# Kernel tuning notes

Measured on AMD Instinct MI355X. Metric: run time of the kernel, lower is better.

Reference implementation:

```python
import jax, jax.numpy as jnp
import numpy as np

C = 1024          # embed_dim
H = 16            # num_heads
D = C // H        # head_dim = 64
M = 64            # memory_size
HID = 4 * C       # mlp hidden
EPS = 1e-5


def _ln(x, g, b):
    mu = jnp.mean(x, axis=-1, keepdims=True)
    var = jnp.mean(jnp.square(x - mu), axis=-1, keepdims=True)
    return (x - mu) * jax.lax.rsqrt(var + EPS) * g + b


def setup_inputs() -> dict:
    key = jax.random.key(0)
    ks = jax.random.split(key, 16)
    s = 0.02
    return {
        'x': jax.random.normal(ks[0], (2, 2048, C), jnp.float32),
        'memory': jax.random.normal(ks[1], (1, M, C), jnp.float32),
        'ln1_g': jnp.ones((C,), jnp.float32),
        'ln1_b': jnp.zeros((C,), jnp.float32),
        'w_qkv': jax.random.normal(ks[2], (C, 3 * C), jnp.float32) * s,
        'b_qkv': jnp.zeros((3 * C,), jnp.float32),
        'w_out': jax.random.normal(ks[3], (C, C), jnp.float32) * s,
        'b_out': jnp.zeros((C,), jnp.float32),
        'w_mem': jax.random.normal(ks[4], (C, C), jnp.float32) * s,
        'b_mem': jnp.zeros((C,), jnp.float32),
        'ln2_g': jnp.ones((C,), jnp.float32),
        'ln2_b': jnp.zeros((C,), jnp.float32),
        'w_fc1': jax.random.normal(ks[5], (C, HID), jnp.float32) * s,
        'b_fc1': jnp.zeros((HID,), jnp.float32),
        'w_fc2': jax.random.normal(ks[6], (HID, C), jnp.float32) * s,
        'b_fc2': jnp.zeros((C,), jnp.float32),
    }


def reference(x, memory, ln1_g, ln1_b, w_qkv, b_qkv, w_out, b_out,
              w_mem, b_mem, ln2_g, ln2_b, w_fc1, b_fc1, w_fc2, b_fc2):
    B, T, _ = x.shape
    scale = 1.0 / np.sqrt(D)

    # --- InfiniAttention on norm1(x) ---
    h = _ln(x, ln1_g, ln1_b)
    qkv = (h @ w_qkv + b_qkv).reshape(B, T, 3, H, D)
    q = qkv[:, :, 0].transpose(0, 2, 1, 3)  # (B,H,T,D)
    k = qkv[:, :, 1].transpose(0, 2, 1, 3)
    v = qkv[:, :, 2].transpose(0, 2, 1, 3)

    # local full softmax attention over the window of T tokens
    attn = jax.nn.softmax(jnp.einsum('bhtd,bhsd->bhts', q, k) * scale, axis=-1)
    local_out = jnp.einsum('bhts,bhsd->bhtd', attn, v)

    # compressive memory read: mem acts as both K and V
    mem = (memory @ w_mem + b_mem)                 # (1,M,C)
    mem_kv = jnp.broadcast_to(mem, (B, M, C)).reshape(B, M, H, D).transpose(0, 2, 1, 3)  # (B,H,M,D)
    mem_attn = jax.nn.softmax(jnp.einsum('bhtd,bhmd->bhtm', q, mem_kv) * scale, axis=-1)
    mem_out = jnp.einsum('bhtm,bhmd->bhtd', mem_attn, mem_kv)

    out = (local_out + mem_out).transpose(0, 2, 1, 3).reshape(B, T, C)
    out = out @ w_out + b_out
    x = x + out

    # --- MLP on norm2(x) ---
    h2 = _ln(x, ln2_g, ln2_b)
    h2 = jax.nn.gelu(h2 @ w_fc1 + b_fc1, approximate=False)
    x = x + h2 @ w_fc2 + b_fc2
    return x
```

## Files before the change

kernel.cpp:

```cpp
#include <hip/hip_runtime.h>
#include <hip/hip_bf16.h>

typedef unsigned short u16;
typedef unsigned int u32;
typedef short bf16x8 __attribute__((ext_vector_type(8)));
typedef float f32x4 __attribute__((ext_vector_type(4)));

__device__ __forceinline__ u16 f2bf(float x) {
    u32 u = __float_as_uint(x);
    u32 rounding = 0x7FFFu + ((u >> 16) & 1u);
    return (u16)((u + rounding) >> 16);
}

__device__ __forceinline__ void gload_lds16(const u16* g, u16* l) {
    __builtin_amdgcn_global_load_lds((const __attribute__((address_space(1))) void*)g,
                                     (__attribute__((address_space(3))) void*)l, 16, 0, 0);
}

__global__ __launch_bounds__(256) void ln_kernel(const float* __restrict__ in,
                                                 const float* __restrict__ g,
                                                 const float* __restrict__ b,
                                                 u16* __restrict__ outp) {
    int tok = blockIdx.x;
    int t = threadIdx.x;
    const float4* row = (const float4*)(in + (size_t)tok * 1024);
    float4 v = row[t];
    float s = v.x + v.y + v.z + v.w;
    float sq = v.x * v.x + v.y * v.y + v.z * v.z + v.w * v.w;
#pragma unroll
    for (int off = 32; off >= 1; off >>= 1) {
        s += __shfl_xor(s, off);
        sq += __shfl_xor(sq, off);
    }
    __shared__ float rs[4], rq[4];
    int lane = t & 63, w = t >> 6;
    if (lane == 0) { rs[w] = s; rq[w] = sq; }
    __syncthreads();
    s = rs[0] + rs[1] + rs[2] + rs[3];
    sq = rq[0] + rq[1] + rq[2] + rq[3];
    float mean = s * (1.0f / 1024.0f);
    float var = sq * (1.0f / 1024.0f) - mean * mean;
    float rstd = rsqrtf(var + 1e-5f);
    float4 gg = ((const float4*)g)[t];
    float4 bb = ((const float4*)b)[t];
    u16* o = outp + (size_t)tok * 1024 + t * 4;
    o[0] = f2bf((v.x - mean) * rstd * gg.x + bb.x);
    o[1] = f2bf((v.y - mean) * rstd * gg.y + bb.y);
    o[2] = f2bf((v.z - mean) * rstd * gg.z + bb.z);
    o[3] = f2bf((v.w - mean) * rstd * gg.w + bb.w);
}

__global__ __launch_bounds__(256) void transpose_w(const float* __restrict__ W,
                                                   u16* __restrict__ WT, int K, int N) {
    __shared__ float tile[32][33];
    int n0 = blockIdx.x * 32, k0 = blockIdx.y * 32;
    int tx = threadIdx.x & 31, ty = threadIdx.x >> 5;
#pragma unroll
    for (int i = 0; i < 4; i++) {
        int kk = ty + i * 8;
        tile[kk][tx] = W[(size_t)(k0 + kk) * N + n0 + tx];
    }
    __syncthreads();
#pragma unroll
    for (int i = 0; i < 4; i++) {
        int nn = ty + i * 8;
        WT[(size_t)(n0 + nn) * K + k0 + tx] = f2bf(tile[tx][nn]);
    }
}

__global__ void convert_bf(const float* __restrict__ in, u16* __restrict__ outp, int n) {
    int i = blockIdx.x * blockDim.x + threadIdx.x;
    if (i < n) outp[i] = f2bf(in[i]);
}

template <int MODE, int BM>
__global__ __launch_bounds__(256) void gemm_bf16(const u16* A, const u16* BT,
                                                 const float* __restrict__ bias,
                                                 const float* res, void* outv,
                                                 int M, int N, int K) {
    __shared__ __align__(16) u16 As[BM * 32];
    __shared__ __align__(16) u16 Bs[128 * 32];
    constexpr int MI = BM / 32;
    int rowBase = blockIdx.y * BM, colBase = blockIdx.x * 128;
    int t = threadIdx.x, lane = t & 63, w = t >> 6;
    int wr = w >> 1, wc = w & 1, r = lane & 15, g = lane >> 4;

    int lrow = lane >> 2;
    int scol = (lane & 3) * 8;
    const u16* b0 = BT + (size_t)(colBase + (w * 2 + 0) * 16 + lrow) * K + scol;
    const u16* b1 = BT + (size_t)(colBase + (w * 2 + 1) * 16 + lrow) * K + scol;
    u16* lB0 = &Bs[(w * 2 + 0) * 512];
    u16* lB1 = &Bs[(w * 2 + 1) * 512];
    const u16* a0;
    const u16* a1 = nullptr;
    u16 *lA0, *lA1 = nullptr;
    if constexpr (BM == 128) {
        a0 = A + (size_t)(rowBase + (w * 2 + 0) * 16 + lrow) * K + scol;
        a1 = A + (size_t)(rowBase + (w * 2 + 1) * 16 + lrow) * K + scol;
        lA0 = &As[(w * 2 + 0) * 512];
        lA1 = &As[(w * 2 + 1) * 512];
    } else {
        a0 = A + (size_t)(rowBase + w * 16 + lrow) * K + scol;
        lA0 = &As[w * 512];
    }

    f32x4 acc[MI][4] = {};

    for (int k0 = 0; k0 < K; k0 += 32) {
        __syncthreads();
        gload_lds16(a0 + k0, lA0);
        if constexpr (BM == 128) gload_lds16(a1 + k0, lA1);
        gload_lds16(b0 + k0, lB0);
        gload_lds16(b1 + k0, lB1);
        __syncthreads();
        bf16x8 af[MI], bfr[4];
#pragma unroll
        for (int mi = 0; mi < MI; mi++)
            af[mi] = *(const bf16x8*)&As[(wr * (BM / 2) + mi * 16 + r) * 32 + g * 8];
#pragma unroll
        for (int ni = 0; ni < 4; ni++)
            bfr[ni] = *(const bf16x8*)&Bs[(wc * 64 + ni * 16 + r) * 32 + g * 8];
#pragma unroll
        for (int mi = 0; mi < MI; mi++)
#pragma unroll
            for (int ni = 0; ni < 4; ni++)
                acc[mi][ni] = __builtin_amdgcn_mfma_f32_16x16x32_bf16(af[mi], bfr[ni], acc[mi][ni], 0, 0, 0);
    }

#pragma unroll
    for (int mi = 0; mi < MI; mi++) {
#pragma unroll
        for (int ni = 0; ni < 4; ni++) {
#pragma unroll
            for (int rr = 0; rr < 4; rr++) {
                int grow = rowBase + wr * (BM / 2) + mi * 16 + g * 4 + rr;
                int gcol = colBase + wc * 64 + ni * 16 + r;
                if (grow < M) {
                    float v = acc[mi][ni][rr] + bias[gcol];
                    if constexpr (MODE == 1) {
                        v = 0.5f * v * (1.0f + erff(v * 0.70710678118f));
                    }
                    if constexpr (MODE == 2) {
                        ((float*)outv)[(size_t)grow * N + gcol] = v + res[(size_t)grow * N + gcol];
                    } else {
                        ((u16*)outv)[(size_t)grow * N + gcol] = f2bf(v);
                    }
                }
            }
        }
    }
}

__global__ __launch_bounds__(256) void attn_kernel(const u16* __restrict__ qkv,
                                                   const u16* __restrict__ memkv,
                                                   u16* __restrict__ outp) {
    __shared__ __align__(16) u16 K_lds[64][72];
    __shared__ __align__(16) u32 P32[64][36];
    __shared__ __align__(16) u32 VT32[64][36];
    const int T = 2048, C3 = 3072;
    int qt = blockIdx.x, bh = blockIdx.y;
    int b = bh >> 4, h = bh & 15;
    int t0 = qt * 64;
    int tid = threadIdx.x, lane = tid & 63, w = tid >> 6, r = lane & 15, g = lane >> 4;
    size_t qkvb = (size_t)b * T * C3;

    const u16* qrow = qkv + qkvb + (size_t)(t0 + w * 16 + r) * C3 + h * 64;
    bf16x8 aq0 = *(const bf16x8*)(qrow + g * 8);
    bf16x8 aq1 = *(const bf16x8*)(qrow + 32 + g * 8);
#pragma unroll
    for (int i = 0; i < 8; i++) {
        float f0 = __uint_as_float(((u32)(u16)aq0[i]) << 16) * 0.18033688f;
        float f1 = __uint_as_float(((u32)(u16)aq1[i]) << 16) * 0.18033688f;
        aq0[i] = (short)f2bf(f0);
        aq1[i] = (short)f2bf(f1);
    }

    int s_row = tid >> 3;
    int s_col = (tid & 7) << 3;
    int v_d = tid & 63;
    int v_u = tid >> 6;

    f32x4 O[4] = {};
    float m_[4] = {-1e30f, -1e30f, -1e30f, -1e30f};
    float lv[4] = {0.f, 0.f, 0.f, 0.f};

    struct VRegs { uint4 k0, k1; u32 va[8]; };

    auto load_tile = [&](const u16* Kb2, size_t Kstr, const u16* Vb2, size_t Vstr) {
        VRegs R;
        R.k0 = *(const uint4*)&Kb2[Kstr * s_row + s_col];
        R.k1 = *(const uint4*)&Kb2[Kstr * (s_row + 32) + s_col];
        const u16* vp = Vb2 + v_d;
#pragma unroll
        for (int j = 0; j < 4; j++) {
            int rv = (j < 2) ? (2 * v_u + j) : (8 + 2 * v_u + (j - 2));
            R.va[2 * j] = (u32)vp[(size_t)rv * Vstr] | ((u32)vp[(size_t)(rv + 16) * Vstr] << 16);
            R.va[2 * j + 1] = (u32)vp[(size_t)(rv + 32) * Vstr] | ((u32)vp[(size_t)(rv + 48) * Vstr] << 16);
        }
        return R;
    };
    auto write_tile = [&](const VRegs& R) {
        *(uint4*)&K_lds[s_row][s_col] = R.k0;
        *(uint4*)&K_lds[s_row + 32][s_col] = R.k1;
        uint4 w0, w1;
        w0.x = R.va[0]; w0.y = R.va[1]; w0.z = R.va[2]; w0.w = R.va[3];
        w1.x = R.va[4]; w1.y = R.va[5]; w1.z = R.va[6]; w1.w = R.va[7];
        *(uint4*)&VT32[v_d][4 * v_u] = w0;
        *(uint4*)&VT32[v_d][16 + 4 * v_u] = w1;
    };

    auto compute_tile = [&]() {
        f32x4 sv[4];
#pragma unroll
        for (int n = 0; n < 4; n++) {
            bf16x8 bk0 = *(const bf16x8*)&K_lds[n * 16 + r][g * 8];
            bf16x8 bk1 = *(const bf16x8*)&K_lds[n * 16 + r][32 + g * 8];
            f32x4 z = {0.f, 0.f, 0.f, 0.f};
            z = __builtin_amdgcn_mfma_f32_16x16x32_bf16(aq0, bk0, z, 0, 0, 0);
            z = __builtin_amdgcn_mfma_f32_16x16x32_bf16(aq1, bk1, z, 0, 0, 0);
            sv[n] = z;
        }
        float mxl[4];
#pragma unroll
        for (int rr = 0; rr < 4; rr++)
            mxl[rr] = fmaxf(fmaxf(sv[0][rr], sv[1][rr]), fmaxf(sv[2][rr], sv[3][rr]));
        float dmax = fmaxf(fmaxf(mxl[0] - m_[0], mxl[1] - m_[1]),
                           fmaxf(mxl[2] - m_[2], mxl[3] - m_[3]));
        if (!__all(dmax <= 8.0f)) {
#pragma unroll
            for (int rr = 0; rr < 4; rr++) {
                float mxr = mxl[rr];
#pragma unroll
                for (int off = 8; off >= 1; off >>= 1) mxr = fmaxf(mxr, __shfl_xor(mxr, off));
                float mn = fmaxf(m_[rr], mxr);
                float alpha = exp2f(m_[rr] - mn);
                m_[rr] = mn;
                lv[rr] *= alpha;
#pragma unroll
                for (int n = 0; n < 4; n++) O[n][rr] *= alpha;
            }
        }
#pragma unroll
        for (int rr = 0; rr < 4; rr++) {
            float p0 = exp2f(sv[0][rr] - m_[rr]);
            float p1 = exp2f(sv[1][rr] - m_[rr]);
            float p2 = exp2f(sv[2][rr] - m_[rr]);
            float p3 = exp2f(sv[3][rr] - m_[rr]);
            lv[rr] += (p0 + p1) + (p2 + p3);
            uint2 pw;
            pw.x = __builtin_amdgcn_perm(__float_as_uint(p1), __float_as_uint(p0), 0x07060302u);
            pw.y = __builtin_amdgcn_perm(__float_as_uint(p3), __float_as_uint(p2), 0x07060302u);
            *(uint2*)&P32[w * 16 + g * 4 + rr][2 * r] = pw;
        }
        bf16x8 ap0 = *(const bf16x8*)&P32[w * 16 + r][4 * g];
        bf16x8 ap1 = *(const bf16x8*)&P32[w * 16 + r][16 + 4 * g];
#pragma unroll
        for (int n = 0; n < 4; n++) {
            bf16x8 bv0 = *(const bf16x8*)&VT32[n * 16 + r][4 * g];
            bf16x8 bv1 = *(const bf16x8*)&VT32[n * 16 + r][16 + 4 * g];
            O[n] = __builtin_amdgcn_mfma_f32_16x16x32_bf16(ap0, bv0, O[n], 0, 0, 0);
            O[n] = __builtin_amdgcn_mfma_f32_16x16x32_bf16(ap1, bv1, O[n], 0, 0, 0);
        }
    };

    const u16* Kb = qkv + qkvb + 1024 + h * 64;
    const u16* Vb = qkv + qkvb + 2048 + h * 64;
    VRegs R = load_tile(Kb, C3, Vb, C3);
    for (int t = 0; t < 32; t++) {
        __syncthreads();
        write_tile(R);
        __syncthreads();
        if (t < 31)
            R = load_tile(Kb + (size_t)(t + 1) * 64 * C3, C3, Vb + (size_t)(t + 1) * 64 * C3, C3);
        else
            R = load_tile(memkv + h * 64, 1024, memkv + h * 64, 1024);
        compute_tile();
    }
    float outLocal[4][4];
#pragma unroll
    for (int rr = 0; rr < 4; rr++) {
        float ls = lv[rr];
#pragma unroll
        for (int off = 8; off >= 1; off >>= 1) ls += __shfl_xor(ls, off);
        float inv = 1.0f / ls;
#pragma unroll
        for (int n = 0; n < 4; n++) outLocal[n][rr] = O[n][rr] * inv;
    }
#pragma unroll
    for (int n = 0; n < 4; n++) { f32x4 z = {0.f, 0.f, 0.f, 0.f}; O[n] = z; }
#pragma unroll
    for (int rr = 0; rr < 4; rr++) { m_[rr] = -1e30f; lv[rr] = 0.f; }
    __syncthreads();
    write_tile(R);
    __syncthreads();
    compute_tile();
#pragma unroll
    for (int rr = 0; rr < 4; rr++) {
        float ls = lv[rr];
#pragma unroll
        for (int off = 8; off >= 1; off >>= 1) ls += __shfl_xor(ls, off);
        float inv = 1.0f / ls;
        int row = t0 + w * 16 + g * 4 + rr;
#pragma unroll
        for (int n = 0; n < 4; n++) {
            float v2 = outLocal[n][rr] + O[n][rr] * inv;
            outp[((size_t)(b * T + row)) * 1024 + h * 64 + n * 16 + r] = f2bf(v2);
        }
    }
}

extern "C" void kernel_launch(void* const* d_in, const int* in_sizes, int n_in,
                              void* d_out, int out_size, void* d_ws, size_t ws_size,
                              hipStream_t stream) {
    const float* x      = (const float*)d_in[0];
    const float* memory = (const float*)d_in[1];
    const float* ln1_g  = (const float*)d_in[2];
    const float* ln1_b  = (const float*)d_in[3];
    const float* w_qkv  = (const float*)d_in[4];
    const float* b_qkv  = (const float*)d_in[5];
    const float* w_out  = (const float*)d_in[6];
    const float* b_out  = (const float*)d_in[7];
    const float* w_mem  = (const float*)d_in[8];
    const float* b_mem  = (const float*)d_in[9];
    const float* ln2_g  = (const float*)d_in[10];
    const float* ln2_b  = (const float*)d_in[11];
    const float* w_fc1  = (const float*)d_in[12];
    const float* b_fc1  = (const float*)d_in[13];
    const float* w_fc2  = (const float*)d_in[14];
    const float* b_fc2  = (const float*)d_in[15];
    float* out = (float*)d_out;

    char* ws = (char*)d_ws;
    size_t off = 0;
    auto alloc = [&](size_t bytes) { size_t o = off; off += (bytes + 255) & ~(size_t)255; return o; };
    u16* h_bf    = (u16*)(ws + alloc((size_t)4096 * 1024 * 2));
    u16* qkv_bf  = (u16*)(ws + alloc((size_t)4096 * 3072 * 2));
    u16* attn_bf = (u16*)(ws + alloc((size_t)4096 * 1024 * 2));
    u16* g1_bf   = (u16*)(ws + alloc((size_t)4096 * 4096 * 2));
    u16* mem_bf  = (u16*)(ws + alloc((size_t)64 * 1024 * 2));
    u16* memA_bf = (u16*)(ws + alloc((size_t)64 * 1024 * 2));
    u16* wqkvT   = (u16*)(ws + alloc((size_t)3072 * 1024 * 2));
    u16* woutT   = (u16*)(ws + alloc((size_t)1024 * 1024 * 2));
    u16* wmemT   = (u16*)(ws + alloc((size_t)1024 * 1024 * 2));
    u16* wfc1T   = (u16*)(ws + alloc((size_t)4096 * 1024 * 2));
    u16* wfc2T   = (u16*)(ws + alloc((size_t)1024 * 4096 * 2));

    transpose_w<<<dim3(3072 / 32, 1024 / 32), 256, 0, stream>>>(w_qkv, wqkvT, 1024, 3072);
    transpose_w<<<dim3(1024 / 32, 1024 / 32), 256, 0, stream>>>(w_out, woutT, 1024, 1024);
    transpose_w<<<dim3(1024 / 32, 1024 / 32), 256, 0, stream>>>(w_mem, wmemT, 1024, 1024);
    transpose_w<<<dim3(4096 / 32, 1024 / 32), 256, 0, stream>>>(w_fc1, wfc1T, 1024, 4096);
    transpose_w<<<dim3(1024 / 32, 4096 / 32), 256, 0, stream>>>(w_fc2, wfc2T, 4096, 1024);
    convert_bf<<<dim3(256), 256, 0, stream>>>(memory, memA_bf, 64 * 1024);

    ln_kernel<<<dim3(4096), 256, 0, stream>>>(x, ln1_g, ln1_b, h_bf);

    gemm_bf16<0, 128><<<dim3(24, 32), 256, 0, stream>>>(h_bf, wqkvT, b_qkv, nullptr, qkv_bf, 4096, 3072, 1024);

    gemm_bf16<0, 64><<<dim3(8, 1), 256, 0, stream>>>(memA_bf, wmemT, b_mem, nullptr, mem_bf, 64, 1024, 1024);

    attn_kernel<<<dim3(32, 32), 256, 0, stream>>>(qkv_bf, mem_bf, attn_bf);

    gemm_bf16<2, 64><<<dim3(8, 64), 256, 0, stream>>>(attn_bf, woutT, b_out, x, out, 4096, 1024, 1024);

    ln_kernel<<<dim3(4096), 256, 0, stream>>>(out, ln2_g, ln2_b, h_bf);

    gemm_bf16<1, 128><<<dim3(32, 32), 256, 0, stream>>>(h_bf, wfc1T, b_fc1, nullptr, g1_bf, 4096, 4096, 1024);

    gemm_bf16<2, 64><<<dim3(8, 64), 256, 0, stream>>>(g1_bf, wfc2T, b_fc2, out, out, 4096, 1024, 4096);

    (void)in_sizes; (void)n_in; (void)out_size; (void)ws_size;
}
```

Measured before the change: 524.2 us.

## Pre-tile K/V into swizzled layout and double-buffer attention via direct LDS loads

Adds a prep_kv kernel that rewrites K and transposed V (and the memory K/V) into per-tile, XOR-swizzled 64x64 blocks, stored in the unused fc1 buffer. The attention kernel then stages each tile with global_load_lds into double-buffered LDS, removing the register round trip and the strided 2-byte V gathers. It also swizzles P and drops one barrier per iteration. An XCD-aware block remap is applied to the GEMMs and attention for L2 locality. The cost is an extra pass over K/V and extra launches.

```diff
diff --git a/kernel.cpp b/kernel.cpp
--- a/kernel.cpp
+++ b/kernel.cpp
@@ -15,6 +15,12 @@
 __device__ __forceinline__ void gload_lds16(const u16* g, u16* l) {
     __builtin_amdgcn_global_load_lds((const __attribute__((address_space(1))) void*)g,
                                      (__attribute__((address_space(3))) void*)l, 16, 0, 0);
+}
+
+__device__ __forceinline__ int xcd_swz(int id, int nwg) {
+    int q = nwg >> 3, r = nwg & 7;
+    int x = id & 7, k = id >> 3;
+    return (x < r ? x * (q + 1) : r * (q + 1) + (x - r) * q) + k;
 }
 
 __global__ __launch_bounds__(256) void ln_kernel(const float* __restrict__ in,
@@ -73,6 +79,40 @@
     if (i < n) outp[i] = f2bf(in[i]);
 }
 
+__global__ __launch_bounds__(256) void prep_kv(const u16* __restrict__ src,
+                                               u32* __restrict__ kdst, u32* __restrict__ vdst,
+                                               long bstride, int rstride, int koff, int voff) {
+    int t = blockIdx.x, bh = blockIdx.y;
+    int b = bh >> 4, h = bh & 15;
+    int tid = threadIdx.x;
+    const u16* kS = src + (size_t)b * bstride + (size_t)(t * 64) * rstride + koff + h * 64;
+    const u16* vS = src + (size_t)b * bstride + (size_t)(t * 64) * rstride + voff + h * 64;
+    u32* kD = kdst + ((size_t)bh * gridDim.x + t) * 2048;
+    u32* vD = vdst + ((size_t)bh * gridDim.x + t) * 2048;
+#pragma unroll
+    for (int c = 0; c < 2; c++) {
+        int idx = tid + c * 256;
+        int row = idx >> 3, blk = idx & 7;
+        uint4 q = *(const uint4*)&kS[(size_t)row * rstride + blk * 8];
+        *(uint4*)&kD[row * 32 + ((blk ^ (row & 7)) << 2)] = q;
+    }
+#pragma unroll
+    for (int c = 0; c < 2; c++) {
+        int idx = tid + c * 256;
+        int drow = idx >> 3, kblk = idx & 7;
+        u32 vv[4];
+#pragma unroll
+        for (int e = 0; e < 4; e++) {
+            int j0 = kblk * 8 + 2 * e, j1 = j0 + 1;
+            int kv0 = 16 * (j0 & 3) + (j0 >> 2);
+            int kv1 = 16 * (j1 & 3) + (j1 >> 2);
+            vv[e] = (u32)vS[(size_t)kv0 * rstride + drow] |
+                    ((u32)vS[(size_t)kv1 * rstride + drow] << 16);
+        }
+        *(uint4*)&vD[drow * 32 + ((kblk ^ (drow & 7)) << 2)] = *(uint4*)vv;
+    }
+}
+
 template <int MODE, int BM>
 __global__ __launch_bounds__(256) void gemm_bf16(const u16* A, const u16* BT,
                                                  const float* __restrict__ bias,
@@ -81,7 +121,11 @@
     __shared__ __align__(16) u16 As[BM * 32];
     __shared__ __align__(16) u16 Bs[128 * 32];
     constexpr int MI = BM / 32;
-    int rowBase = blockIdx.y * BM, colBase = blockIdx.x * 128;
+    int gx = gridDim.x, gy = gridDim.y;
+    int id = blockIdx.y * gx + blockIdx.x;
+    int id2 = xcd_swz(id, gx * gy);
+    int bx = id2 / gy, by = id2 % gy;
+    int rowBase = by * BM, colBase = bx * 128;
     int t = threadIdx.x, lane = t & 63, w = t >> 6;
     int wr = w >> 1, wc = w & 1, r = lane & 15, g = lane >> 4;
 
@@ -152,16 +196,22 @@
 }
 
 __global__ __launch_bounds__(256) void attn_kernel(const u16* __restrict__ qkv,
-                                                   const u16* __restrict__ memkv,
+                                                   const u32* __restrict__ ktiled,
+                                                   const u32* __restrict__ vttiled,
+                                                   const u32* __restrict__ memK,
+                                                   const u32* __restrict__ memVT,
                                                    u16* __restrict__ outp) {
-    __shared__ __align__(16) u16 K_lds[64][72];
-    __shared__ __align__(16) u32 P32[64][36];
-    __shared__ __align__(16) u32 VT32[64][36];
+    __shared__ __align__(16) u32 KB[2][2048];
+    __shared__ __align__(16) u32 VB[2][2048];
+    __shared__ __align__(16) u32 P32[64][32];
     const int T = 2048, C3 = 3072;
-    int qt = blockIdx.x, bh = blockIdx.y;
+    int id = blockIdx.y * 32 + blockIdx.x;
+    int id2 = xcd_swz(id, 1024);
+    int bh = id2 >> 5, qt = id2 & 31;
     int b = bh >> 4, h = bh & 15;
     int t0 = qt * 64;
     int tid = threadIdx.x, lane = tid & 63, w = tid >> 6, r = lane & 15, g = lane >> 4;
+    int swz = r & 7;
     size_t qkvb = (size_t)b * T * C3;
 
     const u16* qrow = qkv + qkvb + (size_t)(t0 + w * 16 + r) * C3 + h * 64;
@@ -175,46 +225,32 @@
         aq1[i] = (short)f2bf(f1);
     }
 
-    int s_row = tid >> 3;
-    int s_col = (tid & 7) << 3;
-    int v_d = tid & 63;
-    int v_u = tid >> 6;
-
     f32x4 O[4] = {};
     float m_[4] = {-1e30f, -1e30f, -1e30f, -1e30f};
     float lv[4] = {0.f, 0.f, 0.f, 0.f};
 
-    struct VRegs { uint4 k0, k1; u32 va[8]; };
-
-    auto load_tile = [&](const u16* Kb2, size_t Kstr, const u16* Vb2, size_t Vstr) {
-        VRegs R;
-        R.k0 = *(const uint4*)&Kb2[Kstr * s_row + s_col];
-        R.k1 = *(const uint4*)&Kb2[Kstr * (s_row + 32) + s_col];
-        const u16* vp = Vb2 + v_d;
-#pragma unroll
-        for (int j = 0; j < 4; j++) {
-            int rv = (j < 2) ? (2 * v_u + j) : (8 + 2 * v_u + (j - 2));
-            R.va[2 * j] = (u32)vp[(size_t)rv * Vstr] | ((u32)vp[(size_t)(rv + 16) * Vstr] << 16);
-            R.va[2 * j + 1] = (u32)vp[(size_t)(rv + 32) * Vstr] | ((u32)vp[(size_t)(rv + 48) * Vstr] << 16);
-        }
-        return R;
+    auto stage = [&](int t, int buf) {
+        const u32 *kb, *vb;
+        if (t < 32) {
+            kb = ktiled + ((size_t)bh * 32 + t) * 2048;
+            vb = vttiled + ((size_t)bh * 32 + t) * 2048;
+        } else {
+            kb = memK + (size_t)h * 2048;
+            vb = memVT + (size_t)h * 2048;
+        }
+        gload_lds16((const u16*)(kb + tid * 4), (u16*)&KB[buf][tid * 4]);
+        gload_lds16((const u16*)(kb + 1024 + tid * 4), (u16*)&KB[buf][1024 + tid * 4]);
+        gload_lds16((const u16*)(vb + tid * 4), (u16*)&VB[buf][tid * 4]);
+        gload_lds16((const u16*)(vb + 1024 + tid * 4), (u16*)&VB[buf][1024 + tid * 4]);
     };
-    auto write_tile = [&](const VRegs& R) {
-        *(uint4*)&K_lds[s_row][s_col] = R.k0;
-        *(uint4*)&K_lds[s_row + 32][s_col] = R.k1;
-        uint4 w0, w1;
-        w0.x = R.va[0]; w0.y = R.va[1]; w0.z = R.va[2]; w0.w = R.va[3];
-        w1.x = R.va[4]; w1.y = R.va[5]; w1.z = R.va[6]; w1.w = R.va[7];
-        *(uint4*)&VT32[v_d][4 * v_u] = w0;
-        *(uint4*)&VT32[v_d][16 + 4 * v_u] = w1;
-    };
-
-    auto compute_tile = [&]() {
+
+    auto compute = [&](int buf) {
         f32x4 sv[4];
 #pragma unroll
         for (int n = 0; n < 4; n++) {
-            bf16x8 bk0 = *(const bf16x8*)&K_lds[n * 16 + r][g * 8];
-            bf16x8 bk1 = *(const bf16x8*)&K_lds[n * 16 + r][32 + g * 8];
+            int row = n * 16 + r;
+            bf16x8 bk0 = *(const bf16x8*)&KB[buf][row * 32 + ((g ^ swz) << 2)];
+            bf16x8 bk1 = *(const bf16x8*)&KB[buf][row * 32 + (((4 + g) ^ swz) << 2)];
             f32x4 z = {0.f, 0.f, 0.f, 0.f};
             z = __builtin_amdgcn_mfma_f32_16x16x32_bf16(aq0, bk0, z, 0, 0, 0);
             z = __builtin_amdgcn_mfma_f32_16x16x32_bf16(aq1, bk1, z, 0, 0, 0);
@@ -242,6 +278,7 @@
         }
 #pragma unroll
         for (int rr = 0; rr < 4; rr++) {
+            int q = w * 16 + g * 4 + rr;
             float p0 = exp2f(sv[0][rr] - m_[rr]);
             float p1 = exp2f(sv[1][rr] - m_[rr]);
             float p2 = exp2f(sv[2][rr] - m_[rr]);
@@ -250,50 +287,43 @@
             uint2 pw;
             pw.x = __builtin_amdgcn_perm(__float_as_uint(p1), __float_as_uint(p0), 0x07060302u);
             pw.y = __builtin_amdgcn_perm(__float_as_uint(p3), __float_as_uint(p2), 0x07060302u);
-            *(uint2*)&P32[w * 16 + g * 4 + rr][2 * r] = pw;
-        }
-        bf16x8 ap0 = *(const bf16x8*)&P32[w * 16 + r][4 * g];
-        bf16x8 ap1 = *(const bf16x8*)&P32[w * 16 + r][16 + 4 * g];
+            *(uint2*)&P32[q][4 * ((r >> 1) ^ (q & 7)) + 2 * (r & 1)] = pw;
+        }
+        bf16x8 ap0 = *(const bf16x8*)&P32[w * 16 + r][(g ^ swz) << 2];
+        bf16x8 ap1 = *(const bf16x8*)&P32[w * 16 + r][((4 + g) ^ swz) << 2];
 #pragma unroll
         for (int n = 0; n < 4; n++) {
-            bf16x8 bv0 = *(const bf16x8*)&VT32[n * 16 + r][4 * g];
-            bf16x8 bv1 = *(const bf16x8*)&VT32[n * 16 + r][16 + 4 * g];
+            int row = n * 16 + r;
+            bf16x8 bv0 = *(const bf16x8*)&VB[buf][row * 32 + ((g ^ swz) << 2)];
+            bf16x8 bv1 = *(const bf16x8*)&VB[buf][row * 32 + (((4 + g) ^ swz) << 2)];
             O[n] = __builtin_amdgcn_mfma_f32_16x16x32_bf16(ap0, bv0, O[n], 0, 0, 0);
             O[n] = __builtin_amdgcn_mfma_f32_16x16x32_bf16(ap1, bv1, O[n], 0, 0, 0);
         }
     };
 
-    const u16* Kb = qkv + qkvb + 1024 + h * 64;
-    const u16* Vb = qkv + qkvb + 2048 + h * 64;
-    VRegs R = load_tile(Kb, C3, Vb, C3);
-    for (int t = 0; t < 32; t++) {
+    float outLocal[4][4];
+    stage(0, 0);
+    __syncthreads();
+    for (int tt = 0; tt <= 32; tt++) {
+        if (tt < 32) stage(tt + 1, (tt + 1) & 1);
+        if (tt == 32) {
+#pragma unroll
+            for (int rr = 0; rr < 4; rr++) {
+                float ls = lv[rr];
+#pragma unroll
+                for (int off = 8; off >= 1; off >>= 1) ls += __shfl_xor(ls, off);
+                float inv = 1.0f / ls;
+#pragma unroll
+                for (int n = 0; n < 4; n++) outLocal[n][rr] = O[n][rr] * inv;
+                m_[rr] = -1e30f;
+                lv[rr] = 0.f;
+            }
+#pragma unroll
+            for (int n = 0; n < 4; n++) { f32x4 z = {0.f, 0.f, 0.f, 0.f}; O[n] = z; }
+        }
+        compute(tt & 1);
         __syncthreads();
-        write_tile(R);
-        __syncthreads();
-        if (t < 31)
-            R = load_tile(Kb + (size_t)(t + 1) * 64 * C3, C3, Vb + (size_t)(t + 1) * 64 * C3, C3);
-        else
-            R = load_tile(memkv + h * 64, 1024, memkv + h * 64, 1024);
-        compute_tile();
-    }
-    float outLocal[4][4];
-#pragma unroll
-    for (int rr = 0; rr < 4; rr++) {
-        float ls = lv[rr];
-#pragma unroll
-        for (int off = 8; off >= 1; off >>= 1) ls += __shfl_xor(ls, off);
-        float inv = 1.0f / ls;
-#pragma unroll
-        for (int n = 0; n < 4; n++) outLocal[n][rr] = O[n][rr] * inv;
-    }
-#pragma unroll
-    for (int n = 0; n < 4; n++) { f32x4 z = {0.f, 0.f, 0.f, 0.f}; O[n] = z; }
-#pragma unroll
-    for (int rr = 0; rr < 4; rr++) { m_[rr] = -1e30f; lv[rr] = 0.f; }
-    __syncthreads();
-    write_tile(R);
-    __syncthreads();
-    compute_tile();
+    }
 #pragma unroll
     for (int rr = 0; rr < 4; rr++) {
         float ls = lv[rr];
@@ -345,6 +375,11 @@
     u16* wfc1T   = (u16*)(ws + alloc((size_t)4096 * 1024 * 2));
     u16* wfc2T   = (u16*)(ws + alloc((size_t)1024 * 4096 * 2));
 
+    u32* ktiled  = (u32*)g1_bf;
+    u32* vttiled = ktiled + (size_t)1024 * 2048;
+    u32* memK    = vttiled + (size_t)1024 * 2048;
+    u32* memVT   = memK + (size_t)16 * 2048;
+
     transpose_w<<<dim3(3072 / 32, 1024 / 32), 256, 0, stream>>>(w_qkv, wqkvT, 1024, 3072);
     transpose_w<<<dim3(1024 / 32, 1024 / 32), 256, 0, stream>>>(w_out, woutT, 1024, 1024);
     transpose_w<<<dim3(1024 / 32, 1024 / 32), 256, 0, stream>>>(w_mem, wmemT, 1024, 1024);
@@ -358,7 +393,11 @@
 
     gemm_bf16<0, 64><<<dim3(8, 1), 256, 0, stream>>>(memA_bf, wmemT, b_mem, nullptr, mem_bf, 64, 1024, 1024);
 
-    attn_kernel<<<dim3(32, 32), 256, 0, stream>>>(qkv_bf, mem_bf, attn_bf);
+    prep_kv<<<dim3(32, 32), 256, 0, stream>>>(qkv_bf, ktiled, vttiled,
+                                              (long)2048 * 3072, 3072, 1024, 2048);
+    prep_kv<<<dim3(1, 16), 256, 0, stream>>>(mem_bf, memK, memVT, 0, 1024, 0, 0);
+
+    attn_kernel<<<dim3(32, 32), 256, 0, stream>>>(qkv_bf, ktiled, vttiled, memK, memVT, attn_bf);
 
     gemm_bf16<2, 64><<<dim3(8, 64), 256, 0, stream>>>(attn_bf, woutT, b_out, x, out, 4096, 1024, 1024);
 
```

Result: faster. 493.5 us (-5.9%).
